# Optimization experiments

Measured on AMD Instinct MI355X. Metric: run time of the kernel, lower is better.

The kernel has to match this reference:

```python
import jax, jax.numpy as jnp
import numpy as np

NUM_VOCABS = 1024
OUTPUT_DIM = 1024  # enc_dim + dec_dim
ENC_DIM = 512
DEC_DIM = 512


def setup_inputs() -> dict:
    key = jax.random.key(0)
    k1, k2, k3, k4 = jax.random.split(key, 4)
    encoder_output = jax.random.normal(k1, (4, 256, ENC_DIM), dtype=jnp.float32)
    decoder_output = jax.random.normal(k2, (4, 64, DEC_DIM), dtype=jnp.float32)
    # nn.Linear(output_dim, num_vocabs): weight (V, output_dim), bias (V,)
    lim = 1.0 / np.sqrt(OUTPUT_DIM)
    W = jax.random.uniform(k3, (NUM_VOCABS, OUTPUT_DIM), dtype=jnp.float32, minval=-lim, maxval=lim)
    b = jax.random.uniform(k4, (NUM_VOCABS,), dtype=jnp.float32, minval=-lim, maxval=lim)
    return {"encoder_output": encoder_output, "decoder_output": decoder_output, "W": W, "b": b}


def reference(encoder_output, decoder_output, W, b):
    # Faithful to: cat(repeat(enc), repeat(dec)) @ W.T + b -> log_softmax
    # Equivalent efficient form: project enc and dec separately, broadcast-add.
    enc_dim = encoder_output.shape[-1]
    W_enc, W_dec = W[:, :enc_dim], W[:, enc_dim:]
    enc_proj = jnp.einsum('btd,vd->btv', encoder_output, W_enc)  # (B,T,V)
    dec_proj = jnp.einsum('bud,vd->buv', decoder_output, W_dec)  # (B,U,V)
    logits = enc_proj[:, :, None, :] + dec_proj[:, None, :, :] + b  # (B,T,U,V)
    return jax.nn.log_softmax(logits, axis=-1)
```

## Files before the change

kernel.cpp:

```cpp
#include <hip/hip_runtime.h>
#include <hip/hip_bf16.h>
#include <stdint.h>


#define KDIM 512
#define NV   1024
#define WDIM 1024

typedef __attribute__((ext_vector_type(8))) short short8;
typedef __attribute__((ext_vector_type(4))) float f32x4;

__device__ __forceinline__ ushort f2bf(float f) {
    uint32_t u = __float_as_uint(f);
    uint32_t r = (u + 0x7fffu + ((u >> 16) & 1u)) >> 16;
    return (ushort)r;
}

__global__ __launch_bounds__(256) void cvt_all(
        const float* __restrict__ enc, const float* __restrict__ dec,
        const float* __restrict__ W,
        ushort* __restrict__ encb, ushort* __restrict__ decb, ushort* __restrict__ wb) {
    int blk = blockIdx.x;
    const float* src; ushort* dst; int i;
    if (blk < 512)      { src = enc; dst = encb; i = blk * 256 + threadIdx.x; }
    else if (blk < 640) { src = dec; dst = decb; i = (blk - 512) * 256 + threadIdx.x; }
    else                { src = W;   dst = wb;   i = (blk - 640) * 256 + threadIdx.x; }
    f32x4 v = reinterpret_cast<const f32x4*>(src)[i];
    ushort4 h;
    h.x = f2bf(v.x); h.y = f2bf(v.y); h.z = f2bf(v.z); h.w = f2bf(v.w);
    reinterpret_cast<ushort4*>(dst)[i] = h;
}

__global__ __launch_bounds__(256) void gemm_proj(
        const ushort* __restrict__ encA, const ushort* __restrict__ decA,
        const ushort* __restrict__ Wb, const float* __restrict__ bias,
        float* __restrict__ encp, float* __restrict__ decp) {
    int tid = threadIdx.x;
    int lane = tid & 63, wid = tid >> 6;
    int wr = wid >> 1, wc = wid & 1;

    const ushort* A; float* out; int wcol_off, bm; bool use_bias;
    if (blockIdx.y < 16) { A = encA; out = encp; wcol_off = 0;   bm = blockIdx.y * 64;        use_bias = true;  }
    else                 { A = decA; out = decp; wcol_off = 512; bm = (blockIdx.y - 16) * 64; use_bias = false; }
    int bn = blockIdx.x * 64;
    int r16 = lane & 15, kg = lane >> 4;

    const ushort* a0p = A  + (size_t)(bm + wr * 32 + r16) * KDIM + kg * 8;
    const ushort* a1p = a0p + 16 * KDIM;
    const ushort* b0p = Wb + (size_t)(bn + wc * 32 + r16) * WDIM + wcol_off + kg * 8;
    const ushort* b1p = b0p + 16 * WDIM;

    f32x4 acc00 = {}, acc01 = {}, acc10 = {}, acc11 = {};
    #pragma unroll
    for (int ks = 0; ks < KDIM; ks += 32) {
        short8 a0 = *(const short8*)(a0p + ks);
        short8 a1 = *(const short8*)(a1p + ks);
        short8 b0 = *(const short8*)(b0p + ks);
        short8 b1 = *(const short8*)(b1p + ks);
        acc00 = __builtin_amdgcn_mfma_f32_16x16x32_bf16(a0, b0, acc00, 0, 0, 0);
        acc01 = __builtin_amdgcn_mfma_f32_16x16x32_bf16(a0, b1, acc01, 0, 0, 0);
        acc10 = __builtin_amdgcn_mfma_f32_16x16x32_bf16(a1, b0, acc10, 0, 0, 0);
        acc11 = __builtin_amdgcn_mfma_f32_16x16x32_bf16(a1, b1, acc11, 0, 0, 0);
    }

    int mb = bm + wr * 32 + (lane >> 4) * 4;
    int nb = bn + wc * 32 + (lane & 15);
    #pragma unroll
    for (int i = 0; i < 2; ++i) {
        #pragma unroll
        for (int j = 0; j < 2; ++j) {
            f32x4 acc = (i == 0) ? (j == 0 ? acc00 : acc01) : (j == 0 ? acc10 : acc11);
            int n = nb + j * 16;
            float bv = use_bias ? bias[n] : 0.0f;
            #pragma unroll
            for (int r = 0; r < 4; ++r) {
                int m = mb + i * 16 + r;
                out[(size_t)m * NV + n] = acc[r] + bv;
            }
        }
    }
}

__global__ __launch_bounds__(256) void lse_kernel(
        const float* __restrict__ encp, const float* __restrict__ decp,
        float* __restrict__ out) {
    int tid = threadIdx.x;
    int lane = tid & 63;
    int w = blockIdx.x * 4 + (tid >> 6);
    int bt = w >> 3;
    int ug = w & 7;
    int b = bt >> 8;

    const float* ep = encp + (size_t)bt * NV + lane * 4;
    f32x4 e0 = *(const f32x4*)(ep + 0);
    f32x4 e1 = *(const f32x4*)(ep + 256);
    f32x4 e2 = *(const f32x4*)(ep + 512);
    f32x4 e3 = *(const f32x4*)(ep + 768);

    const float* dbase = decp + (size_t)(b << 6) * NV + lane * 4;

    #pragma unroll
    for (int uu = 0; uu < 8; ++uu) {
        int u = ug * 8 + uu;
        const float* dp = dbase + (size_t)u * NV;
        f32x4 d0 = *(const f32x4*)(dp + 0)   + e0;
        f32x4 d1 = *(const f32x4*)(dp + 256) + e1;
        f32x4 d2 = *(const f32x4*)(dp + 512) + e2;
        f32x4 d3 = *(const f32x4*)(dp + 768) + e3;

        float s = __expf(d0.x) + __expf(d0.y) + __expf(d0.z) + __expf(d0.w)
                + __expf(d1.x) + __expf(d1.y) + __expf(d1.z) + __expf(d1.w)
                + __expf(d2.x) + __expf(d2.y) + __expf(d2.z) + __expf(d2.w)
                + __expf(d3.x) + __expf(d3.y) + __expf(d3.z) + __expf(d3.w);
        #pragma unroll
        for (int off = 32; off >= 1; off >>= 1)
            s += __shfl_xor(s, off, 64);
        float lse = __logf(s);

        float* op = out + (size_t)((bt << 6) | u) * NV + lane * 4;
        f32x4 lv = {lse, lse, lse, lse};
        __builtin_nontemporal_store(d0 - lv, (f32x4*)(op + 0));
        __builtin_nontemporal_store(d1 - lv, (f32x4*)(op + 256));
        __builtin_nontemporal_store(d2 - lv, (f32x4*)(op + 512));
        __builtin_nontemporal_store(d3 - lv, (f32x4*)(op + 768));
    }
}

extern "C" void kernel_launch(void* const* d_in, const int* in_sizes, int n_in,
                              void* d_out, int out_size, void* d_ws, size_t ws_size,
                              hipStream_t stream) {
    const float* enc = (const float*)d_in[0];
    const float* dec = (const float*)d_in[1];
    const float* W   = (const float*)d_in[2];
    const float* b   = (const float*)d_in[3];
    float* out = (float*)d_out;

    char* ws = (char*)d_ws;
    float*  encp = (float*)(ws + 0);
    float*  decp = (float*)(ws + 4194304);
    ushort* encb = (ushort*)(ws + 5242880);
    ushort* decb = (ushort*)(ws + 6291456);
    ushort* wb   = (ushort*)(ws + 6553600);

    cvt_all<<<1664, 256, 0, stream>>>(enc, dec, W, encb, decb, wb);
    gemm_proj<<<dim3(16, 20), 256, 0, stream>>>(encb, decb, wb, b, encp, decp);
    lse_kernel<<<2048, 256, 0, stream>>>(encp, decp, out);
}
```

Baseline: 77.44 us.

## Compute log-sum-exp via bf16 MFMA GEMM of exponentiated projections

Uses the identity sum_v exp(e_v + d_v) = exp(E) · exp(D)^T to compute all (t,u) log-sum-exp values as a small bf16 MFMA GEMM over the vocab dimension, then a separate add kernel writes e+d-lse. This removes the per-row transcendental exp work and cross-lane reductions from the bandwidth-bound output pass. It trades that for an extra kernel launch, a GEMM run on only 16 blocks, bf16 rounding of the exponentials, and overflow risk since no max is subtracted. The output stores also change from nontemporal to regular stores.

Result: slower. 100.1 us (+29.3%).

```diff
diff --git a/kernel.cpp b/kernel.cpp
--- a/kernel.cpp
+++ b/kernel.cpp
@@ -81,9 +81,62 @@
     }
 }
 
-__global__ __launch_bounds__(256) void lse_kernel(
+__device__ __forceinline__ short8 exp8(const float* p) {
+    f32x4 lo = *(const f32x4*)p;
+    f32x4 hi = *(const f32x4*)(p + 4);
+    short8 r;
+    r[0] = (short)f2bf(__expf(lo.x)); r[1] = (short)f2bf(__expf(lo.y));
+    r[2] = (short)f2bf(__expf(lo.z)); r[3] = (short)f2bf(__expf(lo.w));
+    r[4] = (short)f2bf(__expf(hi.x)); r[5] = (short)f2bf(__expf(hi.y));
+    r[6] = (short)f2bf(__expf(hi.z)); r[7] = (short)f2bf(__expf(hi.w));
+    return r;
+}
+
+__global__ __launch_bounds__(256) void lse_gemm(
         const float* __restrict__ encp, const float* __restrict__ decp,
-        float* __restrict__ out) {
+        float* __restrict__ lse_tab) {
+    int tid = threadIdx.x;
+    int lane = tid & 63, wid = tid >> 6;
+    int wr = wid >> 1, wc = wid & 1;
+    int bm = blockIdx.x * 64;
+    int b  = blockIdx.x >> 2;
+    int r16 = lane & 15, kg = lane >> 4;
+
+    const float* a0p = encp + (size_t)(bm + wr * 32 + r16) * NV + kg * 8;
+    const float* a1p = a0p + 16 * NV;
+    const float* b0p = decp + (size_t)((b << 6) + wc * 32 + r16) * NV + kg * 8;
+    const float* b1p = b0p + 16 * NV;
+
+    f32x4 acc00 = {}, acc01 = {}, acc10 = {}, acc11 = {};
+    for (int ks = 0; ks < NV; ks += 32) {
+        short8 a0 = exp8(a0p + ks);
+        short8 a1 = exp8(a1p + ks);
+        short8 b0 = exp8(b0p + ks);
+        short8 b1 = exp8(b1p + ks);
+        acc00 = __builtin_amdgcn_mfma_f32_16x16x32_bf16(a0, b0, acc00, 0, 0, 0);
+        acc01 = __builtin_amdgcn_mfma_f32_16x16x32_bf16(a0, b1, acc01, 0, 0, 0);
+        acc10 = __builtin_amdgcn_mfma_f32_16x16x32_bf16(a1, b0, acc10, 0, 0, 0);
+        acc11 = __builtin_amdgcn_mfma_f32_16x16x32_bf16(a1, b1, acc11, 0, 0, 0);
+    }
+
+    int mb = bm + wr * 32 + (lane >> 4) * 4;
+    int nb = wc * 32 + (lane & 15);
+    #pragma unroll
+    for (int i = 0; i < 2; ++i) {
+        #pragma unroll
+        for (int j = 0; j < 2; ++j) {
+            f32x4 acc = (i == 0) ? (j == 0 ? acc00 : acc01) : (j == 0 ? acc10 : acc11);
+            int n = nb + j * 16;
+            #pragma unroll
+            for (int r = 0; r < 4; ++r)
+                lse_tab[(size_t)(mb + i * 16 + r) * 64 + n] = __logf(acc[r]);
+        }
+    }
+}
+
+__global__ __launch_bounds__(256) void add_kernel(
+        const float* __restrict__ encp, const float* __restrict__ decp,
+        const float* __restrict__ lse_tab, float* __restrict__ out) {
     int tid = threadIdx.x;
     int lane = tid & 63;
     int w = blockIdx.x * 4 + (tid >> 6);
@@ -98,31 +151,24 @@
     f32x4 e3 = *(const f32x4*)(ep + 768);
 
     const float* dbase = decp + (size_t)(b << 6) * NV + lane * 4;
+    const float* lbase = lse_tab + ((size_t)bt << 6);
 
     #pragma unroll
     for (int uu = 0; uu < 8; ++uu) {
         int u = ug * 8 + uu;
+        float lse = lbase[u];
+        f32x4 lv = {lse, lse, lse, lse};
         const float* dp = dbase + (size_t)u * NV;
-        f32x4 d0 = *(const f32x4*)(dp + 0)   + e0;
-        f32x4 d1 = *(const f32x4*)(dp + 256) + e1;
-        f32x4 d2 = *(const f32x4*)(dp + 512) + e2;
-        f32x4 d3 = *(const f32x4*)(dp + 768) + e3;
-
-        float s = __expf(d0.x) + __expf(d0.y) + __expf(d0.z) + __expf(d0.w)
-                + __expf(d1.x) + __expf(d1.y) + __expf(d1.z) + __expf(d1.w)
-                + __expf(d2.x) + __expf(d2.y) + __expf(d2.z) + __expf(d2.w)
-                + __expf(d3.x) + __expf(d3.y) + __expf(d3.z) + __expf(d3.w);
-        #pragma unroll
-        for (int off = 32; off >= 1; off >>= 1)
-            s += __shfl_xor(s, off, 64);
-        float lse = __logf(s);
+        f32x4 o0 = *(const f32x4*)(dp + 0)   + e0 - lv;
+        f32x4 o1 = *(const f32x4*)(dp + 256) + e1 - lv;
+        f32x4 o2 = *(const f32x4*)(dp + 512) + e2 - lv;
+        f32x4 o3 = *(const f32x4*)(dp + 768) + e3 - lv;
 
         float* op = out + (size_t)((bt << 6) | u) * NV + lane * 4;
-        f32x4 lv = {lse, lse, lse, lse};
-        __builtin_nontemporal_store(d0 - lv, (f32x4*)(op + 0));
-        __builtin_nontemporal_store(d1 - lv, (f32x4*)(op + 256));
-        __builtin_nontemporal_store(d2 - lv, (f32x4*)(op + 512));
-        __builtin_nontemporal_store(d3 - lv, (f32x4*)(op + 768));
+        *(f32x4*)(op + 0)   = o0;
+        *(f32x4*)(op + 256) = o1;
+        *(f32x4*)(op + 512) = o2;
+        *(f32x4*)(op + 768) = o3;
     }
 }
 
@@ -141,8 +187,10 @@
     ushort* encb = (ushort*)(ws + 5242880);
     ushort* decb = (ushort*)(ws + 6291456);
     ushort* wb   = (ushort*)(ws + 6553600);
+    float*  lset = (float*)(ws + 8650752);
 
     cvt_all<<<1664, 256, 0, stream>>>(enc, dec, W, encb, decb, wb);
     gemm_proj<<<dim3(16, 20), 256, 0, stream>>>(encb, decb, wb, b, encp, decp);
-    lse_kernel<<<2048, 256, 0, stream>>>(encp, decp, out);
+    lse_gemm<<<16, 256, 0, stream>>>(encp, decp, lset);
+    add_kernel<<<2048, 256, 0, stream>>>(encp, decp, lset, out);
 }
```
